# Kernel optimization log

Measured on AMD Instinct MI355X. Metric: run time of the kernel, lower is better.

## Reference

```python
import jax, jax.numpy as jnp
import numpy as np

N_NODES = 4096
D_MODEL = 1024
MAX_DEPS = 8
N_CLASSES = 64


def setup_inputs() -> dict:
    key = jax.random.key(0)
    k1, k2, k3 = jax.random.split(key, 3)
    questions = jax.random.normal(k1, (N_NODES, D_MODEL), dtype=jnp.float32)
    # Padded dependency lists; every dependency index is strictly < node index,
    # so processing nodes in index order is a valid topological order.
    rng = np.random.default_rng(0)
    dep_idx = np.zeros((N_NODES, MAX_DEPS), dtype=np.int32)
    dep_mask = np.zeros((N_NODES, MAX_DEPS), dtype=np.int32)
    for i in range(1, N_NODES):
        nd = int(rng.integers(1, MAX_DEPS + 1))
        dep_idx[i, :nd] = rng.integers(0, i, size=nd)
        dep_mask[i, :nd] = 1
    W1 = jax.random.normal(k2, (D_MODEL, 2 * D_MODEL), dtype=jnp.float32) * 0.02
    b1 = jnp.zeros((D_MODEL,), dtype=jnp.float32)
    W2 = jax.random.normal(k3, (N_CLASSES, D_MODEL), dtype=jnp.float32) * 0.02
    b2 = jnp.zeros((N_CLASSES,), dtype=jnp.float32)
    return {
        "questions": questions,
        "W1": W1,
        "b1": b1,
        "W2": W2,
        "b2": b2,
        "dep_idx": jnp.asarray(dep_idx),
        "dep_mask": jnp.asarray(dep_mask),
    }


def reference(questions, W1, b1, W2, b2, dep_idx, dep_mask):
    n_nodes, d_model = questions.shape

    def step(answers, xs):
        i, q, deps, mask = xs
        ctx = answers[deps]                       # [MAX_DEPS, d_model] gather
        m = mask.astype(q.dtype)
        # masked mean; all-zero mask -> zero context (matches torch zeros branch)
        ctx_mean = (ctx * m[:, None]).sum(0) / jnp.maximum(m.sum(), 1.0)
        combined = jnp.concatenate([q, ctx_mean])  # [2*d_model]
        h = jax.nn.gelu(combined @ W1.T + b1, approximate=False)
        return answers.at[i].set(h), None

    answers0 = jnp.zeros((n_nodes, d_model), dtype=questions.dtype)
    xs = (jnp.arange(n_nodes), questions, dep_idx, dep_mask)
    answers, _ = jax.lax.scan(step, answers0, xs)
    root_answer = answers[n_nodes - 1]            # root = last node in topo order
    return root_answer @ W2.T + b2                # [n_classes] logits
```

## Files before the change

kernel.cpp:

```cpp
#include <hip/hip_runtime.h>

#define NN 4096
#define DM 1024
#define MD 8
#define NW 256
#define NCOL 4
#define NT 512
#define NWAVE (NT / 64)
#define UR 4
#define MAXL 4097

#define MI_NLEV 0
#define MI_ROOTPOS 1
#define MI_ARRIVE 8
#define MI_LO 1024
#define MI_NL 6144
#define MI_NU 10240
#define MI_PERM 14336
#define MI_DCNT 18432
#define MI_INV 22528
#define MI_DPOS 26624

typedef __attribute__((ext_vector_type(8))) short bf16x8;
typedef __attribute__((ext_vector_type(8))) unsigned short ushort8;
typedef __attribute__((ext_vector_type(4))) float f32x4;

__device__ __forceinline__ float gelu_f(float x) {
  return 0.5f * x * (1.0f + erff(x * 0.70710678118654752440f));
}
__device__ __forceinline__ unsigned short f2bf(float x) {
  unsigned int u = __builtin_bit_cast(unsigned int, x);
  u += 0x7FFFu + ((u >> 16) & 1u);
  return (unsigned short)(u >> 16);
}
__device__ __forceinline__ float bf2f(unsigned short v) {
  return __builtin_bit_cast(float, (unsigned int)v << 16);
}

__global__ __launch_bounds__(1024) void k_pro(
    const float* __restrict__ Q, const int* __restrict__ dep_idx,
    const int* __restrict__ dep_mask, int* __restrict__ meta,
    unsigned short* __restrict__ Qb) {
  __shared__ int lvl[NN];
  __shared__ int liv[NN];
  __shared__ int mcl[NN];
  __shared__ int cnt[3 * NN];
  __shared__ int pos[NN];
  __shared__ int s_changed, s_max;
  const int t = threadIdx.x;

  if (blockIdx.x != 0) {
    const size_t total = (size_t)NN * DM / 8;
    for (size_t c = (size_t)(blockIdx.x - 1) * 1024 + t; c < total; c += 255 * 1024) {
      const size_t i = c * 8;
      float4 a = *(const float4*)&Q[i];
      float4 b = *(const float4*)&Q[i + 4];
      ushort8 o;
      o[0] = f2bf(a.x); o[1] = f2bf(a.y); o[2] = f2bf(a.z); o[3] = f2bf(a.w);
      o[4] = f2bf(b.x); o[5] = f2bf(b.y); o[6] = f2bf(b.z); o[7] = f2bf(b.w);
      *(ushort8*)&Qb[i] = o;
    }
    return;
  }

  for (int i = t; i < NN; i += 1024) {
    lvl[i] = 0; liv[i] = (i == NN - 1) ? 1 : 0; mcl[i] = 0x7FFFFFFF;
  }
  for (int i = t; i < 3 * NN; i += 1024) cnt[i] = 0;
  if (t == 0) s_max = 0;
  __syncthreads();

  for (int u = 0; u < 4; ++u) {
    const int i = u * 1024 + t;
    const int4 d0 = *(const int4*)&dep_idx[i * MD];
    const int4 d1 = *(const int4*)&dep_idx[i * MD + 4];
    const int4 m0 = *(const int4*)&dep_mask[i * MD];
    const int4 m1 = *(const int4*)&dep_mask[i * MD + 4];
    int my = 0;
    for (;;) {
      if (t == 0) s_changed = 0;
      __syncthreads();
      int m = 0;
      if (m0.x) { int l = lvl[d0.x] + 1; m = m > l ? m : l; }
      if (m0.y) { int l = lvl[d0.y] + 1; m = m > l ? m : l; }
      if (m0.z) { int l = lvl[d0.z] + 1; m = m > l ? m : l; }
      if (m0.w) { int l = lvl[d0.w] + 1; m = m > l ? m : l; }
      if (m1.x) { int l = lvl[d1.x] + 1; m = m > l ? m : l; }
      if (m1.y) { int l = lvl[d1.y] + 1; m = m > l ? m : l; }
      if (m1.z) { int l = lvl[d1.z] + 1; m = m > l ? m : l; }
      if (m1.w) { int l = lvl[d1.w] + 1; m = m > l ? m : l; }
      if (m > my) { my = m; lvl[i] = m; s_changed = 1; }
      __syncthreads();
      if (!s_changed) break;
    }
  }
  for (int u = 3; u >= 0; --u) {
    const int i = u * 1024 + t;
    const int4 d0 = *(const int4*)&dep_idx[i * MD];
    const int4 d1 = *(const int4*)&dep_idx[i * MD + 4];
    const int4 m0 = *(const int4*)&dep_mask[i * MD];
    const int4 m1 = *(const int4*)&dep_mask[i * MD + 4];
    for (;;) {
      if (t == 0) s_changed = 0;
      __syncthreads();
      bool ch = false;
      if (liv[i]) {
        if (m0.x && !liv[d0.x]) { liv[d0.x] = 1; ch = true; }
        if (m0.y && !liv[d0.y]) { liv[d0.y] = 1; ch = true; }
        if (m0.z && !liv[d0.z]) { liv[d0.z] = 1; ch = true; }
        if (m0.w && !liv[d0.w]) { liv[d0.w] = 1; ch = true; }
        if (m1.x && !liv[d1.x]) { liv[d1.x] = 1; ch = true; }
        if (m1.y && !liv[d1.y]) { liv[d1.y] = 1; ch = true; }
        if (m1.z && !liv[d1.z]) { liv[d1.z] = 1; ch = true; }
        if (m1.w && !liv[d1.w]) { liv[d1.w] = 1; ch = true; }
      }
      if (ch) s_changed = 1;
      __syncthreads();
      if (!s_changed) break;
    }
  }
  for (int i = t; i < NN; i += 1024) {
    if (!liv[i]) continue;
    const int4 d0 = *(const int4*)&dep_idx[i * MD];
    const int4 d1 = *(const int4*)&dep_idx[i * MD + 4];
    const int4 m0 = *(const int4*)&dep_mask[i * MD];
    const int4 m1 = *(const int4*)&dep_mask[i * MD + 4];
    const int L = lvl[i];
    if (m0.x) atomicMin(&mcl[d0.x], L);
    if (m0.y) atomicMin(&mcl[d0.y], L);
    if (m0.z) atomicMin(&mcl[d0.z], L);
    if (m0.w) atomicMin(&mcl[d0.w], L);
    if (m1.x) atomicMin(&mcl[d1.x], L);
    if (m1.y) atomicMin(&mcl[d1.y], L);
    if (m1.z) atomicMin(&mcl[d1.z], L);
    if (m1.w) atomicMin(&mcl[d1.w], L);
  }
  __syncthreads();
  for (int i = t; i < NN; i += 1024) {
    const int key = liv[i] ? ((mcl[i] == lvl[i] + 1) ? 0 : 1) : 2;
    mcl[i] = key;
    atomicAdd(&cnt[3 * lvl[i] + key], 1);
    atomicMax(&s_max, lvl[i]);
  }
  __syncthreads();
  const int nL = s_max + 1;
  if (t == 0) {
    int off = 0;
    for (int l = 0; l < nL; ++l) {
      meta[MI_LO + l] = off;
      const int a = cnt[3 * l], b = cnt[3 * l + 1], c = cnt[3 * l + 2];
      meta[MI_NU + l] = a;
      meta[MI_NL + l] = a + b;
      cnt[3 * l] = off; off += a;
      cnt[3 * l + 1] = off; off += b;
      cnt[3 * l + 2] = off; off += c;
    }
    meta[MI_LO + nL] = off;
    meta[MI_NLEV] = nL;
  }
  __syncthreads();
  for (int i = t; i < NN; i += 1024)
    pos[i] = atomicAdd(&cnt[3 * lvl[i] + mcl[i]], 1);
  __syncthreads();
  for (int i = t; i < NN; i += 1024) {
    const int r = pos[i];
    meta[MI_PERM + r] = i;
    const int4 d0 = *(const int4*)&dep_idx[i * MD];
    const int4 d1 = *(const int4*)&dep_idx[i * MD + 4];
    const int4 m0 = *(const int4*)&dep_mask[i * MD];
    const int4 m1 = *(const int4*)&dep_mask[i * MD + 4];
    const int dd[8] = {d0.x, d0.y, d0.z, d0.w, d1.x, d1.y, d1.z, d1.w};
    const int mm[8] = {m0.x, m0.y, m0.z, m0.w, m1.x, m1.y, m1.z, m1.w};
    int nd = 0;
    #pragma unroll
    for (int k = 0; k < MD; ++k)
      if (mm[k]) { meta[MI_DPOS + r * MD + nd] = pos[dd[k]]; ++nd; }
    for (int k = nd; k < MD; ++k) meta[MI_DPOS + r * MD + k] = 0;
    meta[MI_DCNT + r] = nd;
    ((float*)meta)[MI_INV + r] = nd ? 1.0f / (float)nd : 0.0f;
  }
  if (t == 0) meta[MI_ROOTPOS] = pos[NN - 1];
  for (int i = t; i < NW; i += 1024) meta[MI_ARRIVE + i] = 0;
}

__global__ __launch_bounds__(256) void k_preq(
    const unsigned short* __restrict__ Qb, const float* __restrict__ W1,
    const float* __restrict__ b1, float* __restrict__ preQ) {
  const int t = threadIdx.x;
  const int wave = t >> 6, lane = t & 63;
  const int wm = wave >> 1, wn = wave & 1;
  const int m0 = blockIdx.y * 128 + wm * 64;
  const int n0 = blockIdx.x * 128 + wn * 64;
  const int lrow = lane & 15;
  const int klo = (lane >> 4) * 8;
  f32x4 acc[4][4] = {};
  for (int k0 = 0; k0 < DM; k0 += 32) {
    bf16x8 af[4];
    #pragma unroll
    for (int f = 0; f < 4; ++f)
      af[f] = *(const bf16x8*)&Qb[(size_t)(m0 + f * 16 + lrow) * DM + k0 + klo];
    bf16x8 bfr[4];
    #pragma unroll
    for (int g = 0; g < 4; ++g) {
      const float* wsrc = &W1[(size_t)(n0 + g * 16 + lrow) * 2048 + k0 + klo];
      float4 w0 = *(const float4*)&wsrc[0];
      float4 w1 = *(const float4*)&wsrc[4];
      bf16x8 bb;
      bb[0] = (short)f2bf(w0.x); bb[1] = (short)f2bf(w0.y);
      bb[2] = (short)f2bf(w0.z); bb[3] = (short)f2bf(w0.w);
      bb[4] = (short)f2bf(w1.x); bb[5] = (short)f2bf(w1.y);
      bb[6] = (short)f2bf(w1.z); bb[7] = (short)f2bf(w1.w);
      bfr[g] = bb;
    }
    #pragma unroll
    for (int f = 0; f < 4; ++f)
      #pragma unroll
      for (int g = 0; g < 4; ++g)
        acc[f][g] = __builtin_amdgcn_mfma_f32_16x16x32_bf16(af[f], bfr[g], acc[f][g], 0, 0, 0);
  }
  float b1v[4];
  #pragma unroll
  for (int g = 0; g < 4; ++g) b1v[g] = b1[n0 + g * 16 + lrow];
  const int mrow = (lane >> 4) * 4;
  #pragma unroll
  for (int f = 0; f < 4; ++f)
    #pragma unroll
    for (int g = 0; g < 4; ++g) {
      const int n = n0 + g * 16 + lrow;
      #pragma unroll
      for (int r = 0; r < 4; ++r)
        preQ[(size_t)(m0 + f * 16 + mrow + r) * DM + n] = acc[f][g][r] + b1v[g];
    }
}

__global__ __launch_bounds__(NT) void k_levels(
    const float* __restrict__ W1, const float* __restrict__ preQ,
    unsigned short* __restrict__ hPb, float4* __restrict__ gPan, int* __restrict__ meta,
    const float* __restrict__ W2, const float* __restrict__ b2, float* __restrict__ out) {
  const int tid = threadIdx.x;
  const int wb = blockIdx.x;
  const int c0 = wb * NCOL;
  const int wave = tid >> 6, lane = tid & 63;
  const int nL = meta[MI_NLEV];
  const int rootRow = meta[MI_ROOTPOS];
  __shared__ int s_lo[MAXL];
  __shared__ int s_nl[MAXL];
  __shared__ int s_nu[MAXL];
  __shared__ float4 preLDS[NT];
  for (int i = tid; i <= nL; i += NT) s_lo[i] = meta[MI_LO + i];
  for (int i = tid; i < nL; i += NT) { s_nl[i] = meta[MI_NL + i]; s_nu[i] = meta[MI_NU + i]; }
  float4 wreg[NCOL][4];
  #pragma unroll
  for (int cc = 0; cc < NCOL; ++cc)
    #pragma unroll
    for (int q = 0; q < 4; ++q)
      wreg[cc][q] = *(const float4*)&W1[(size_t)(c0 + cc) * 2048 + 1024 + lane * 16 + q * 4];
  __syncthreads();
  float4* gp = gPan + (size_t)wb * NN;
  const float* invA = (const float*)&meta[MI_INV];

  auto bphase = [&](int rlo, int rhi) {
    for (int base = rlo + wave * UR; base < rhi; base += NWAVE * UR) {
      const int cnt = rhi - base;
      ushort8 hv[UR][2];
      #pragma unroll
      for (int u = 0; u < UR; ++u) {
        const int r = base + ((u < cnt) ? u : 0);
        const ushort8* h8 = (const ushort8*)&hPb[(size_t)r * DM];
        hv[u][0] = h8[lane * 2];
        hv[u][1] = h8[lane * 2 + 1];
      }
      float rr[UR][NCOL];
      #pragma unroll
      for (int u = 0; u < UR; ++u) {
        float hf[16];
        #pragma unroll
        for (int e = 0; e < 8; ++e) { hf[e] = bf2f(hv[u][0][e]); hf[8 + e] = bf2f(hv[u][1][e]); }
        #pragma unroll
        for (int cc = 0; cc < NCOL; ++cc) {
          float a = 0.f;
          #pragma unroll
          for (int q = 0; q < 4; ++q)
            a += hf[q * 4 + 0] * wreg[cc][q].x + hf[q * 4 + 1] * wreg[cc][q].y
               + hf[q * 4 + 2] * wreg[cc][q].z + hf[q * 4 + 3] * wreg[cc][q].w;
          rr[u][cc] = a;
        }
      }
      #pragma unroll
      for (int off = 1; off < 64; off <<= 1)
        #pragma unroll
        for (int u = 0; u < UR; ++u)
          #pragma unroll
          for (int cc = 0; cc < NCOL; ++cc)
            rr[u][cc] += __shfl_xor(rr[u][cc], off);
      if (lane == 0) {
        #pragma unroll
        for (int u = 0; u < UR; ++u)
          if (u < cnt) gp[base + u] = make_float4(rr[u][0], rr[u][1], rr[u][2], rr[u][3]);
      }
    }
  };

  int plo = 0, pnu = 0, pnl = 0;
  for (int l = 0; l < nL; ++l) {
    const int lo = s_lo[l];
    const int nl = s_nl[l];
    const int nu = s_nu[l];

    for (int r = lo + tid; r < lo + nl; r += NT) {
      const int node = meta[MI_PERM + r];
      const int nd = meta[MI_DCNT + r];
      const float iv = invA[r];
      const int4 p0 = *(const int4*)&meta[MI_DPOS + r * MD];
      const int4 p1 = *(const int4*)&meta[MI_DPOS + r * MD + 4];
      const int dps[8] = {p0.x, p0.y, p0.z, p0.w, p1.x, p1.y, p1.z, p1.w};
      float sx = 0.f, sy = 0.f, sz = 0.f, sw = 0.f;
      #pragma unroll
      for (int d = 0; d < MD; ++d) {
        float4 v = gp[dps[d]];
        sx += (d < nd) ? v.x : 0.f;
        sy += (d < nd) ? v.y : 0.f;
        sz += (d < nd) ? v.z : 0.f;
        sw += (d < nd) ? v.w : 0.f;
      }
      const float4 pq = (l > 0 && r == lo + tid) ? preLDS[tid]
                                                 : *(const float4*)&preQ[(size_t)node * DM + c0];
      const unsigned short h0 = f2bf(gelu_f(pq.x + sx * iv));
      const unsigned short h1 = f2bf(gelu_f(pq.y + sy * iv));
      const unsigned short h2 = f2bf(gelu_f(pq.z + sz * iv));
      const unsigned short h3 = f2bf(gelu_f(pq.w + sw * iv));
      const unsigned long long u = (unsigned long long)h0 | ((unsigned long long)h1 << 16)
                                 | ((unsigned long long)h2 << 32) | ((unsigned long long)h3 << 48);
      __hip_atomic_store((unsigned long long*)&hPb[(size_t)r * DM + c0], u,
                         __ATOMIC_RELAXED, __HIP_MEMORY_SCOPE_AGENT);
    }
    __syncthreads();
    if (tid == 0)
      __hip_atomic_store(&meta[MI_ARRIVE + wb], l + 1, __ATOMIC_RELAXED, __HIP_MEMORY_SCOPE_AGENT);
    if (l + 1 < nL && tid < s_nl[l + 1]) {
      const int node2 = meta[MI_PERM + s_lo[l + 1] + tid];
      preLDS[tid] = *(const float4*)&preQ[(size_t)node2 * DM + c0];
    }
    bphase(plo + pnu, plo + pnl);
    if (tid < 64) {
      for (;;) {
        int m = 1 << 30;
        #pragma unroll
        for (int u = 0; u < 4; ++u) {
          int v = __hip_atomic_load(&meta[MI_ARRIVE + tid * 4 + u], __ATOMIC_RELAXED, __HIP_MEMORY_SCOPE_AGENT);
          m = v < m ? v : m;
        }
        #pragma unroll
        for (int off = 1; off < 64; off <<= 1) {
          int o = __shfl_xor(m, off);
          m = o < m ? o : m;
        }
        if (m >= l + 1) break;
        __builtin_amdgcn_s_sleep(1);
      }
    }
    __syncthreads();
    bphase(lo, lo + nu);
    plo = lo; pnu = nu; pnl = nl;
    __syncthreads();
  }

  if (wb == 0) {
    float* red = (float*)preLDS;
    const int j = tid >> 3, kc = tid & 7;
    const ushort8* h8 = (const ushort8*)&hPb[(size_t)rootRow * DM];
    const float* wr2 = W2 + (size_t)j * DM;
    float acc = 0.f;
    for (int k = kc * 128; k < kc * 128 + 128; k += 8) {
      ushort8 hv = h8[k >> 3];
      float4 wa = *(const float4*)&wr2[k];
      float4 wb4 = *(const float4*)&wr2[k + 4];
      acc += bf2f(hv[0]) * wa.x + bf2f(hv[1]) * wa.y + bf2f(hv[2]) * wa.z + bf2f(hv[3]) * wa.w
           + bf2f(hv[4]) * wb4.x + bf2f(hv[5]) * wb4.y + bf2f(hv[6]) * wb4.z + bf2f(hv[7]) * wb4.w;
    }
    red[tid] = acc;
    __syncthreads();
    if (kc == 0) {
      float s = 0.f;
      #pragma unroll
      for (int e = 0; e < 8; ++e) s += red[j * 8 + e];
      out[j] = s + b2[j];
    }
  }
}

extern "C" void kernel_launch(void* const* d_in, const int* in_sizes, int n_in,
                              void* d_out, int out_size, void* d_ws, size_t ws_size,
                              hipStream_t stream) {
  const float* Q        = (const float*)d_in[0];
  const float* W1       = (const float*)d_in[1];
  const float* b1       = (const float*)d_in[2];
  const float* W2       = (const float*)d_in[3];
  const float* b2       = (const float*)d_in[4];
  const int*   dep_idx  = (const int*)d_in[5];
  const int*   dep_mask = (const int*)d_in[6];

  char* ws = (char*)d_ws;
  float*          preQ = (float*)ws;
  unsigned short* hPb  = (unsigned short*)(ws + (16ull << 20));
  unsigned short* Qb   = (unsigned short*)(ws + (24ull << 20));
  float4*         gPan = (float4*)(ws + (32ull << 20));
  int*            meta = (int*)(ws + (48ull << 20));
  float*          out  = (float*)d_out;

  k_pro<<<dim3(256), dim3(1024), 0, stream>>>(Q, dep_idx, dep_mask, meta, Qb);
  k_preq<<<dim3(DM / 128, NN / 128), dim3(256), 0, stream>>>(Qb, W1, b1, preQ);
  k_levels<<<dim3(NW), dim3(NT), 0, stream>>>(W1, preQ, hPb, gPan, meta, W2, b2, out);
}
```

Before: 536.0 us.

## Drop urgent/deferred split and run full context GEMV after each level barrier

The prologue no longer classifies live nodes by whether their earliest consumer is the very next level, so each level's live nodes form one contiguous block. The level loop drops the deferred b-phase that used to overlap with the inter-block barrier spin. It now computes the context projection for all live nodes of a level after the barrier. This simplifies the metadata and the schedule, but it puts more GEMV work on the critical path after each grid-wide wait and loses the overlap.

```diff
diff --git a/kernel.cpp b/kernel.cpp
--- a/kernel.cpp
+++ b/kernel.cpp
@@ -15,11 +15,10 @@
 #define MI_ARRIVE 8
 #define MI_LO 1024
 #define MI_NL 6144
-#define MI_NU 10240
-#define MI_PERM 14336
-#define MI_DCNT 18432
-#define MI_INV 22528
-#define MI_DPOS 26624
+#define MI_PERM 10240
+#define MI_DCNT 14336
+#define MI_INV 18432
+#define MI_DPOS 22528
 
 typedef __attribute__((ext_vector_type(8))) short bf16x8;
 typedef __attribute__((ext_vector_type(8))) unsigned short ushort8;
@@ -43,8 +42,7 @@
     unsigned short* __restrict__ Qb) {
   __shared__ int lvl[NN];
   __shared__ int liv[NN];
-  __shared__ int mcl[NN];
-  __shared__ int cnt[3 * NN];
+  __shared__ int cnt[2 * NN];
   __shared__ int pos[NN];
   __shared__ int s_changed, s_max;
   const int t = threadIdx.x;
@@ -63,10 +61,8 @@
     return;
   }
 
-  for (int i = t; i < NN; i += 1024) {
-    lvl[i] = 0; liv[i] = (i == NN - 1) ? 1 : 0; mcl[i] = 0x7FFFFFFF;
-  }
-  for (int i = t; i < 3 * NN; i += 1024) cnt[i] = 0;
+  for (int i = t; i < NN; i += 1024) { lvl[i] = 0; liv[i] = (i == NN - 1) ? 1 : 0; }
+  for (int i = t; i < 2 * NN; i += 1024) cnt[i] = 0;
   if (t == 0) s_max = 0;
   __syncthreads();
 
@@ -120,26 +116,7 @@
     }
   }
   for (int i = t; i < NN; i += 1024) {
-    if (!liv[i]) continue;
-    const int4 d0 = *(const int4*)&dep_idx[i * MD];
-    const int4 d1 = *(const int4*)&dep_idx[i * MD + 4];
-    const int4 m0 = *(const int4*)&dep_mask[i * MD];
-    const int4 m1 = *(const int4*)&dep_mask[i * MD + 4];
-    const int L = lvl[i];
-    if (m0.x) atomicMin(&mcl[d0.x], L);
-    if (m0.y) atomicMin(&mcl[d0.y], L);
-    if (m0.z) atomicMin(&mcl[d0.z], L);
-    if (m0.w) atomicMin(&mcl[d0.w], L);
-    if (m1.x) atomicMin(&mcl[d1.x], L);
-    if (m1.y) atomicMin(&mcl[d1.y], L);
-    if (m1.z) atomicMin(&mcl[d1.z], L);
-    if (m1.w) atomicMin(&mcl[d1.w], L);
-  }
-  __syncthreads();
-  for (int i = t; i < NN; i += 1024) {
-    const int key = liv[i] ? ((mcl[i] == lvl[i] + 1) ? 0 : 1) : 2;
-    mcl[i] = key;
-    atomicAdd(&cnt[3 * lvl[i] + key], 1);
+    atomicAdd(&cnt[2 * lvl[i] + (liv[i] ? 0 : 1)], 1);
     atomicMax(&s_max, lvl[i]);
   }
   __syncthreads();
@@ -148,19 +125,17 @@
     int off = 0;
     for (int l = 0; l < nL; ++l) {
       meta[MI_LO + l] = off;
-      const int a = cnt[3 * l], b = cnt[3 * l + 1], c = cnt[3 * l + 2];
-      meta[MI_NU + l] = a;
-      meta[MI_NL + l] = a + b;
-      cnt[3 * l] = off; off += a;
-      cnt[3 * l + 1] = off; off += b;
-      cnt[3 * l + 2] = off; off += c;
+      meta[MI_NL + l] = cnt[2 * l];
+      const int a = cnt[2 * l], b = cnt[2 * l + 1];
+      cnt[2 * l] = off; off += a;
+      cnt[2 * l + 1] = off; off += b;
     }
     meta[MI_LO + nL] = off;
     meta[MI_NLEV] = nL;
   }
   __syncthreads();
   for (int i = t; i < NN; i += 1024)
-    pos[i] = atomicAdd(&cnt[3 * lvl[i] + mcl[i]], 1);
+    pos[i] = atomicAdd(&cnt[2 * lvl[i] + (liv[i] ? 0 : 1)], 1);
   __syncthreads();
   for (int i = t; i < NN; i += 1024) {
     const int r = pos[i];
@@ -245,10 +220,9 @@
   const int rootRow = meta[MI_ROOTPOS];
   __shared__ int s_lo[MAXL];
   __shared__ int s_nl[MAXL];
-  __shared__ int s_nu[MAXL];
   __shared__ float4 preLDS[NT];
   for (int i = tid; i <= nL; i += NT) s_lo[i] = meta[MI_LO + i];
-  for (int i = tid; i < nL; i += NT) { s_nl[i] = meta[MI_NL + i]; s_nu[i] = meta[MI_NU + i]; }
+  for (int i = tid; i < nL; i += NT) s_nl[i] = meta[MI_NL + i];
   float4 wreg[NCOL][4];
   #pragma unroll
   for (int cc = 0; cc < NCOL; ++cc)
@@ -259,55 +233,11 @@
   float4* gp = gPan + (size_t)wb * NN;
   const float* invA = (const float*)&meta[MI_INV];
 
-  auto bphase = [&](int rlo, int rhi) {
-    for (int base = rlo + wave * UR; base < rhi; base += NWAVE * UR) {
-      const int cnt = rhi - base;
-      ushort8 hv[UR][2];
-      #pragma unroll
-      for (int u = 0; u < UR; ++u) {
-        const int r = base + ((u < cnt) ? u : 0);
-        const ushort8* h8 = (const ushort8*)&hPb[(size_t)r * DM];
-        hv[u][0] = h8[lane * 2];
-        hv[u][1] = h8[lane * 2 + 1];
-      }
-      float rr[UR][NCOL];
-      #pragma unroll
-      for (int u = 0; u < UR; ++u) {
-        float hf[16];
-        #pragma unroll
-        for (int e = 0; e < 8; ++e) { hf[e] = bf2f(hv[u][0][e]); hf[8 + e] = bf2f(hv[u][1][e]); }
-        #pragma unroll
-        for (int cc = 0; cc < NCOL; ++cc) {
-          float a = 0.f;
-          #pragma unroll
-          for (int q = 0; q < 4; ++q)
-            a += hf[q * 4 + 0] * wreg[cc][q].x + hf[q * 4 + 1] * wreg[cc][q].y
-               + hf[q * 4 + 2] * wreg[cc][q].z + hf[q * 4 + 3] * wreg[cc][q].w;
-          rr[u][cc] = a;
-        }
-      }
-      #pragma unroll
-      for (int off = 1; off < 64; off <<= 1)
-        #pragma unroll
-        for (int u = 0; u < UR; ++u)
-          #pragma unroll
-          for (int cc = 0; cc < NCOL; ++cc)
-            rr[u][cc] += __shfl_xor(rr[u][cc], off);
-      if (lane == 0) {
-        #pragma unroll
-        for (int u = 0; u < UR; ++u)
-          if (u < cnt) gp[base + u] = make_float4(rr[u][0], rr[u][1], rr[u][2], rr[u][3]);
-      }
-    }
-  };
-
-  int plo = 0, pnu = 0, pnl = 0;
   for (int l = 0; l < nL; ++l) {
     const int lo = s_lo[l];
-    const int nl = s_nl[l];
-    const int nu = s_nu[l];
-
-    for (int r = lo + tid; r < lo + nl; r += NT) {
+    const int nA = s_nl[l];
+
+    for (int r = lo + tid; r < lo + nA; r += NT) {
       const int node = meta[MI_PERM + r];
       const int nd = meta[MI_DCNT + r];
       const float iv = invA[r];
@@ -341,7 +271,6 @@
       const int node2 = meta[MI_PERM + s_lo[l + 1] + tid];
       preLDS[tid] = *(const float4*)&preQ[(size_t)node2 * DM + c0];
     }
-    bphase(plo + pnu, plo + pnl);
     if (tid < 64) {
       for (;;) {
         int m = 1 << 30;
@@ -360,8 +289,46 @@
       }
     }
     __syncthreads();
-    bphase(lo, lo + nu);
-    plo = lo; pnu = nu; pnl = nl;
+
+    for (int base = wave * UR; base < nA; base += NWAVE * UR) {
+      const int cnt = nA - base;
+      ushort8 hv[UR][2];
+      #pragma unroll
+      for (int u = 0; u < UR; ++u) {
+        const int r = lo + base + ((u < cnt) ? u : 0);
+        const ushort8* h8 = (const ushort8*)&hPb[(size_t)r * DM];
+        hv[u][0] = h8[lane * 2];
+        hv[u][1] = h8[lane * 2 + 1];
+      }
+      float rr[UR][NCOL];
+      #pragma unroll
+      for (int u = 0; u < UR; ++u) {
+        float hf[16];
+        #pragma unroll
+        for (int e = 0; e < 8; ++e) { hf[e] = bf2f(hv[u][0][e]); hf[8 + e] = bf2f(hv[u][1][e]); }
+        #pragma unroll
+        for (int cc = 0; cc < NCOL; ++cc) {
+          float a = 0.f;
+          #pragma unroll
+          for (int q = 0; q < 4; ++q)
+            a += hf[q * 4 + 0] * wreg[cc][q].x + hf[q * 4 + 1] * wreg[cc][q].y
+               + hf[q * 4 + 2] * wreg[cc][q].z + hf[q * 4 + 3] * wreg[cc][q].w;
+          rr[u][cc] = a;
+        }
+      }
+      #pragma unroll
+      for (int off = 1; off < 64; off <<= 1)
+        #pragma unroll
+        for (int u = 0; u < UR; ++u)
+          #pragma unroll
+          for (int cc = 0; cc < NCOL; ++cc)
+            rr[u][cc] += __shfl_xor(rr[u][cc], off);
+      if (lane == 0) {
+        #pragma unroll
+        for (int u = 0; u < UR; ++u)
+          if (u < cnt) gp[lo + base + u] = make_float4(rr[u][0], rr[u][1], rr[u][2], rr[u][3]);
+      }
+    }
     __syncthreads();
   }
 
```

After: 487.8 us. 1.1x faster.
